# Optimization experiments

Measured on AMD Instinct MI355X. Metric: run time of the kernel, lower is better.

The kernel has to match this reference:

```python
import jax, jax.numpy as jnp
import numpy as np

N, E, IN_C, HID, OUT_C = 100000, 1600000, 256, 64, 64
K, ALPHA, LN_EPS = 10, 0.1, 1e-5


def _layernorm(h, gamma, beta):
    mu = jnp.mean(h, axis=-1, keepdims=True)
    var = jnp.var(h, axis=-1, keepdims=True)
    return (h - mu) * jax.lax.rsqrt(var + LN_EPS) * gamma + beta


def _appnp(h, edge_index):
    # gcn_norm with added self-loops (fill value 1), symmetric normalization
    n = h.shape[0]
    sl = jnp.arange(n)
    row = jnp.concatenate([edge_index[0], sl])
    col = jnp.concatenate([edge_index[1], sl])
    w = jnp.ones(row.shape[0], dtype=h.dtype)
    deg = jax.ops.segment_sum(w, col, num_segments=n)
    dinv = jnp.where(deg > 0, jax.lax.rsqrt(deg), 0.0)
    norm = dinv[row] * w * dinv[col]  # [E+N]
    h0 = h
    for _ in range(K):
        msg = norm[:, None] * h[row]                       # gather [E+N, HID]
        agg = jax.ops.segment_sum(msg, col, num_segments=n)  # scatter-add
        h = (1.0 - ALPHA) * agg + ALPHA * h0
    return h


def setup_inputs() -> dict:
    key = jax.random.key(0)
    ks = jax.random.split(key, 8)
    x = jax.random.normal(ks[0], (N, IN_C), dtype=jnp.float32)
    edge_index = jax.random.randint(ks[1], (2, E), 0, N, dtype=jnp.int64)
    W1 = jax.random.normal(ks[2], (IN_C, HID), dtype=jnp.float32) / np.sqrt(IN_C)
    b1 = jnp.zeros((HID,), dtype=jnp.float32)
    g1 = jnp.ones((HID,), dtype=jnp.float32)
    be1 = jnp.zeros((HID,), dtype=jnp.float32)
    g2 = jnp.ones((HID,), dtype=jnp.float32)
    be2 = jnp.zeros((HID,), dtype=jnp.float32)
    W2 = jax.random.normal(ks[3], (HID, OUT_C), dtype=jnp.float32) / np.sqrt(HID)
    b2 = jnp.zeros((OUT_C,), dtype=jnp.float32)
    return {"x": x, "edge_index": edge_index, "W1": W1, "b1": b1,
            "g1": g1, "be1": be1, "g2": g2, "be2": be2, "W2": W2, "b2": b2}


def reference(x, edge_index, W1, b1, g1, be1, g2, be2, W2, b2):
    h = jax.nn.gelu(x @ W1 + b1, approximate=False)   # Linear + exact GELU (torch default)
    h = _layernorm(h, g1, be1)
    h = jax.nn.gelu(_appnp(h, edge_index), approximate=False)
    h = _layernorm(h, g2, be2)
    # dropout inactive in eval mode
    return h @ W2 + b2
```

## Files before the change

### kernel.cpp

```cpp
#include <hip/hip_runtime.h>
#include <math.h>

#define HID 64
#define INC 256
#define LN_EPS 1e-5f
#define ALPHA 0.1f
#define NBKT 256
#define BCAP 12288

typedef unsigned short ushort_t;
typedef unsigned int uint_t;
using short8v = __attribute__((ext_vector_type(8))) short;
using float4v = __attribute__((ext_vector_type(4))) float;

__device__ __forceinline__ float gelu_exact(float x) {
    return 0.5f * x * (1.0f + erff(x * 0.70710678118654752f));
}

__device__ __forceinline__ float wave_sum64(float v) {
#pragma unroll
    for (int m = 1; m < 64; m <<= 1) v += __shfl_xor(v, m, 64);
    return v;
}

__device__ __forceinline__ ushort_t f2bf(float f) {
    uint_t u = __float_as_uint(f);
    return (ushort_t)((u + 0x7fffu + ((u >> 16) & 1u)) >> 16);
}
__device__ __forceinline__ float bf_lo(uint_t v) { return __uint_as_float(v << 16); }
__device__ __forceinline__ float bf_hi(uint_t v) { return __uint_as_float(v & 0xffff0000u); }

__device__ __forceinline__ void split_bf(float f, ushort_t& hi, ushort_t& lo) {
    uint_t ub = __float_as_uint(f);
    uint_t h = (ub + 0x7fffu + ((ub >> 16) & 1u)) >> 16;
    hi = (ushort_t)h;
    float fl = f - __uint_as_float(h << 16);
    uint_t lb = __float_as_uint(fl);
    lo = (ushort_t)((lb + 0x7fffu + ((lb >> 16) & 1u)) >> 16);
}

__global__ __launch_bounds__(256) void k_prepW(const float* __restrict__ W1,
                                               ushort_t* __restrict__ whi,
                                               ushort_t* __restrict__ wlo) {
    int e = blockIdx.x * 256 + threadIdx.x;
    int col = e & 63, k = e >> 6;
    float f = W1[(size_t)k * HID + col];
    ushort_t hi, lo;
    split_bf(f, hi, lo);
    int idx = col * 256 + (((k >> 3) ^ (col & 7)) << 3) + (k & 7);
    whi[idx] = hi;
    wlo[idx] = lo;
}

__global__ __launch_bounds__(256) void k_prepW2(const float* __restrict__ W2,
                                                ushort_t* __restrict__ whi,
                                                ushort_t* __restrict__ wlo) {
    int e = blockIdx.x * 256 + threadIdx.x;
    int col = e & 63, k = e >> 6;
    float f = W2[(size_t)k * HID + col];
    ushort_t hi, lo;
    split_bf(f, hi, lo);
    int idx = col * 64 + (((k >> 3) ^ (col & 7)) << 3) + (k & 7);
    whi[idx] = hi;
    wlo[idx] = lo;
}

__global__ __launch_bounds__(256) void k_bin(const int* __restrict__ ei,
                                             int* __restrict__ bcur,
                                             uint_t* __restrict__ binned, int E) {
    __shared__ int hist[NBKT];
    __shared__ int base[NBKT];
    const int t = threadIdx.x;
    const int c0 = blockIdx.x * 4096;
    hist[t] = 0;
    __syncthreads();
#pragma unroll
    for (int i = 0; i < 16; ++i) {
        int e = c0 + i * 256 + t;
        if (e < E) atomicAdd(&hist[ei[E + e] >> 9], 1);
    }
    __syncthreads();
    {
        int h = hist[t];
        base[t] = (h > 0) ? atomicAdd(&bcur[t], h) : 0;
        hist[t] = 0;
    }
    __syncthreads();
#pragma unroll
    for (int i = 0; i < 16; ++i) {
        int e = c0 + i * 256 + t;
        if (e < E) {
            int src = ei[e];
            int dst = ei[E + e];
            int b = dst >> 9;
            int r = atomicAdd(&hist[b], 1);
            int pos = base[b] + r;
            if (pos >= BCAP) pos = BCAP - 1;
            binned[(size_t)b * BCAP + pos] = (uint_t)src | ((uint_t)(dst & 511) << 20);
        }
    }
}

__global__ __launch_bounds__(256) void k_csrA(const uint_t* __restrict__ binned,
                                              const int* __restrict__ bcur,
                                              int* __restrict__ cnt,
                                              float* __restrict__ dinv,
                                              int* __restrict__ offl,
                                              int* __restrict__ bpad, int N) {
    __shared__ int cl[512];
    __shared__ int ps[256];
    const int b = blockIdx.x, t = threadIdx.x;
    const int nE = bcur[b];
    const uint_t* be = binned + (size_t)b * BCAP;
    cl[t] = 0;
    cl[t + 256] = 0;
    __syncthreads();
    for (int i = t; i < nE; i += 256) atomicAdd(&cl[be[i] >> 20], 1);
    __syncthreads();
    const int ca = cl[2 * t], cb = cl[2 * t + 1];
    const int p4a = (ca + 3) & ~3, p4b = (cb + 3) & ~3;
    const int p = p4a + p4b;
    ps[t] = p;
    __syncthreads();
#pragma unroll
    for (int o = 1; o < 256; o <<= 1) {
        int add = (t >= o) ? ps[t - o] : 0;
        __syncthreads();
        ps[t] += add;
        __syncthreads();
    }
    const int pbase = ps[t] - p;
    const int g0 = b * 512 + 2 * t;
    if (g0 < N) {
        cnt[g0] = ca;
        dinv[g0] = rsqrtf((float)(ca + 1));
        offl[g0] = pbase;
    }
    if (g0 + 1 < N) {
        cnt[g0 + 1] = cb;
        dinv[g0 + 1] = rsqrtf((float)(cb + 1));
        offl[g0 + 1] = pbase + p4a;
    }
    if (t == 255) bpad[b] = ps[255];
}

__global__ __launch_bounds__(256) void k_bktscan(const int* __restrict__ bpad,
                                                 int* __restrict__ bbase,
                                                 int* __restrict__ rowstart, int N) {
    __shared__ int s[256];
    const int t = threadIdx.x;
    const int v = bpad[t];
    s[t] = v;
    __syncthreads();
#pragma unroll
    for (int off = 1; off < 256; off <<= 1) {
        int add = (t >= off) ? s[t - off] : 0;
        __syncthreads();
        s[t] += add;
        __syncthreads();
    }
    bbase[t] = s[t] - v;
    if (t == 255) rowstart[N] = s[255];
}

__global__ __launch_bounds__(256) void k_csrB(const uint_t* __restrict__ binned,
                                              const int* __restrict__ bcur,
                                              const int* __restrict__ bbase,
                                              const int* __restrict__ offl,
                                              const int* __restrict__ cnt,
                                              int* __restrict__ csr,
                                              int* __restrict__ rowstart, int N) {
    __shared__ int st[512];
    __shared__ int cur[512];
    const int b = blockIdx.x, t = threadIdx.x;
    const int nE = bcur[b];
    const int gb = bbase[b];
    const uint_t* be = binned + (size_t)b * BCAP;
    const int n0 = b * 512;
    for (int i = t; i < 512; i += 256) {
        int g = n0 + i;
        int s = (g < N) ? gb + offl[g] : 0;
        st[i] = s;
        cur[i] = s;
        if (g < N) rowstart[g] = s;
    }
    __syncthreads();
    for (int i = t; i < nE; i += 256) {
        uint_t rec = be[i];
        int ln = rec >> 20;
        int r = atomicAdd(&cur[ln], 1);
        csr[r] = (int)(rec & 0xFFFFFu);
    }
    __syncthreads();
    for (int i = t; i < 512; i += 256) {
        int g = n0 + i;
        if (g < N) {
            int c = cnt[g];
            int end = st[i] + ((c + 3) & ~3);
            for (int j = st[i] + c; j < end; ++j) csr[j] = N;
        }
    }
}

__global__ __launch_bounds__(512, 4) void k_gemm1ln(const float* __restrict__ x,
                                                    const ushort_t* __restrict__ whi,
                                                    const ushort_t* __restrict__ wlo,
                                                    const float* __restrict__ b1,
                                                    const float* __restrict__ g1,
                                                    const float* __restrict__ be1,
                                                    const float* __restrict__ dinv,
                                                    ushort_t* __restrict__ u0, int N) {
    __shared__ ushort_t Wh[16384];
    __shared__ ushort_t Wl[16384];
    const int t = threadIdx.x;
    {
        const uint4* s1 = (const uint4*)whi;
        uint4* d1 = (uint4*)Wh;
        for (int i = t; i < 2048; i += 512) d1[i] = s1[i];
        const uint4* s2 = (const uint4*)wlo;
        uint4* d2 = (uint4*)Wl;
        for (int i = t; i < 2048; i += 512) d2[i] = s2[i];
    }

    const int lane = t & 63, w = t >> 6;
    const int l15 = lane & 15, lg = lane >> 4;
    const int row0 = blockIdx.x * 128 + w * 16;
    int rowc = row0 + l15;
    if (rowc > N - 1) rowc = N - 1;
    const float* xr = x + (size_t)rowc * INC + lg * 8;

    float4 ax[16];
#pragma unroll
    for (int i = 0; i < 8; ++i) {
        ax[2 * i] = *(const float4*)(xr + i * 32);
        ax[2 * i + 1] = *(const float4*)(xr + i * 32 + 4);
    }
    __syncthreads();

    float4v acc[4];
#pragma unroll
    for (int i = 0; i < 4; ++i) acc[i] = (float4v){0.f, 0.f, 0.f, 0.f};

    union U8 { short8v v; ushort_t u[8]; };

#pragma unroll
    for (int t8 = 0; t8 < 8; ++t8) {
        U8 ahi, alo;
        {
            const float af[8] = {ax[2 * t8].x, ax[2 * t8].y, ax[2 * t8].z, ax[2 * t8].w,
                                 ax[2 * t8 + 1].x, ax[2 * t8 + 1].y, ax[2 * t8 + 1].z,
                                 ax[2 * t8 + 1].w};
#pragma unroll
            for (int j = 0; j < 8; ++j) split_bf(af[j], ahi.u[j], alo.u[j]);
        }
        const int kb = t8 * 4 + lg;
#pragma unroll
        for (int ct = 0; ct < 4; ++ct) {
            const int col = ct * 16 + l15;
            const int idx = col * 256 + ((kb ^ (col & 7)) << 3);
            const short8v bhi = *(const short8v*)&Wh[idx];
            const short8v blo = *(const short8v*)&Wl[idx];
            acc[ct] = __builtin_amdgcn_mfma_f32_16x16x32_bf16(ahi.v, bhi, acc[ct], 0, 0, 0);
            acc[ct] = __builtin_amdgcn_mfma_f32_16x16x32_bf16(ahi.v, blo, acc[ct], 0, 0, 0);
            acc[ct] = __builtin_amdgcn_mfma_f32_16x16x32_bf16(alo.v, bhi, acc[ct], 0, 0, 0);
        }
    }

    float b1c[4], g1c[4], bec[4];
#pragma unroll
    for (int ct = 0; ct < 4; ++ct) {
        const int col = ct * 16 + l15;
        b1c[ct] = b1[col];
        g1c[ct] = g1[col];
        bec[ct] = be1[col];
    }
    float gv[4][4];
#pragma unroll
    for (int ct = 0; ct < 4; ++ct)
#pragma unroll
        for (int r = 0; r < 4; ++r) gv[ct][r] = gelu_exact(acc[ct][r] + b1c[ct]);

    float mu[4], rsv[4];
#pragma unroll
    for (int r = 0; r < 4; ++r) {
        float p = gv[0][r] + gv[1][r] + gv[2][r] + gv[3][r];
        p += __shfl_xor(p, 1, 64);
        p += __shfl_xor(p, 2, 64);
        p += __shfl_xor(p, 4, 64);
        p += __shfl_xor(p, 8, 64);
        mu[r] = p * (1.0f / 64.0f);
        float d0 = gv[0][r] - mu[r], d1 = gv[1][r] - mu[r];
        float d2 = gv[2][r] - mu[r], d3 = gv[3][r] - mu[r];
        float p2 = d0 * d0 + d1 * d1 + d2 * d2 + d3 * d3;
        p2 += __shfl_xor(p2, 1, 64);
        p2 += __shfl_xor(p2, 2, 64);
        p2 += __shfl_xor(p2, 4, 64);
        p2 += __shfl_xor(p2, 8, 64);
        rsv[r] = rsqrtf(p2 * (1.0f / 64.0f) + LN_EPS);
    }
#pragma unroll
    for (int r = 0; r < 4; ++r) {
        const int row = row0 + lg * 4 + r;
        if (row < N) {
            const float di = dinv[row];
#pragma unroll
            for (int ct = 0; ct < 4; ++ct) {
                const float ln = (gv[ct][r] - mu[r]) * rsv[r] * g1c[ct] + bec[ct];
                u0[(size_t)row * HID + ct * 16 + l15] = f2bf(di * ln);
            }
        }
    }
}

__global__ __launch_bounds__(256) void k_prop(const ushort_t* __restrict__ uin,
                                              const ushort_t* __restrict__ u0,
                                              ushort_t* __restrict__ uout,
                                              const int* __restrict__ csr,
                                              const int* __restrict__ rowstart,
                                              const float* __restrict__ dinv, int N) {
    const int t = threadIdx.x;
    const int lane = t & 63;
    const int q = lane >> 4, fl = lane & 15;
    const int node = blockIdx.x * 4 + (t >> 6);
    if (node >= N) return;
    const uint2* U = (const uint2*)uin;
    const int s0 = rowstart[node];
    const int e1 = rowstart[node + 1];
    float a0 = 0.f, a1 = 0.f, a2 = 0.f, a3 = 0.f;
    for (int e = s0; e < e1; e += 16) {
        const int ge = e + 4 * q;
        int4 id = make_int4(N, N, N, N);
        if (ge < e1) id = *(const int4*)(csr + ge);
        const uint2 v0 = U[(size_t)id.x * 16 + fl];
        const uint2 v1 = U[(size_t)id.y * 16 + fl];
        const uint2 v2 = U[(size_t)id.z * 16 + fl];
        const uint2 v3 = U[(size_t)id.w * 16 + fl];
        a0 += bf_lo(v0.x) + bf_lo(v1.x) + bf_lo(v2.x) + bf_lo(v3.x);
        a1 += bf_hi(v0.x) + bf_hi(v1.x) + bf_hi(v2.x) + bf_hi(v3.x);
        a2 += bf_lo(v0.y) + bf_lo(v1.y) + bf_lo(v2.y) + bf_lo(v3.y);
        a3 += bf_hi(v0.y) + bf_hi(v1.y) + bf_hi(v2.y) + bf_hi(v3.y);
    }
    a0 += __shfl_xor(a0, 16, 64); a0 += __shfl_xor(a0, 32, 64);
    a1 += __shfl_xor(a1, 16, 64); a1 += __shfl_xor(a1, 32, 64);
    a2 += __shfl_xor(a2, 16, 64); a2 += __shfl_xor(a2, 32, 64);
    a3 += __shfl_xor(a3, 16, 64); a3 += __shfl_xor(a3, 32, 64);
    if (lane < 16) {
        const uint2 ud = U[(size_t)node * 16 + fl];
        const uint2 uz = ((const uint2*)u0)[(size_t)node * 16 + fl];
        const float di = dinv[node];
        const float c = (1.0f - ALPHA) * di * di;
        const float r0 = c * (a0 + bf_lo(ud.x)) + ALPHA * bf_lo(uz.x);
        const float r1 = c * (a1 + bf_hi(ud.x)) + ALPHA * bf_hi(uz.x);
        const float r2 = c * (a2 + bf_lo(ud.y)) + ALPHA * bf_lo(uz.y);
        const float r3 = c * (a3 + bf_hi(ud.y)) + ALPHA * bf_hi(uz.y);
        uint2 o;
        o.x = (uint_t)f2bf(r0) | ((uint_t)f2bf(r1) << 16);
        o.y = (uint_t)f2bf(r2) | ((uint_t)f2bf(r3) << 16);
        ((uint2*)uout)[(size_t)node * 16 + fl] = o;
    }
}

__global__ __launch_bounds__(256) void k_final(const ushort_t* __restrict__ u,
                                               const int* __restrict__ cnt,
                                               const float* __restrict__ g2,
                                               const float* __restrict__ be2,
                                               const ushort_t* __restrict__ w2hi,
                                               const ushort_t* __restrict__ w2lo,
                                               const float* __restrict__ b2,
                                               float* __restrict__ out, int N) {
    __shared__ ushort_t Wh[4096];
    __shared__ ushort_t Wl[4096];
    const int t = threadIdx.x;
    {
        const uint4* s1 = (const uint4*)w2hi;
        uint4* d1 = (uint4*)Wh;
        for (int i = t; i < 512; i += 256) d1[i] = s1[i];
        const uint4* s2 = (const uint4*)w2lo;
        uint4* d2 = (uint4*)Wl;
        for (int i = t; i < 512; i += 256) d2[i] = s2[i];
    }
    __syncthreads();

    const int lane = t & 63, w = t >> 6;
    const int l15 = lane & 15, lg = lane >> 4;
    const int row0 = blockIdx.x * 64 + w * 16;
    if (row0 >= N) return;
    int rowc = row0 + l15;
    if (rowc > N - 1) rowc = N - 1;

    const uint4 uva = *(const uint4*)(u + (size_t)rowc * HID + lg * 8);
    const uint4 uvb = *(const uint4*)(u + (size_t)rowc * HID + 32 + lg * 8);
    const float sc = sqrtf((float)(cnt[rowc] + 1));

    float v[16];
    {
        const uint_t ua_[4] = {uva.x, uva.y, uva.z, uva.w};
        const uint_t ub_[4] = {uvb.x, uvb.y, uvb.z, uvb.w};
#pragma unroll
        for (int j = 0; j < 4; ++j) {
            v[2 * j] = gelu_exact(bf_lo(ua_[j]) * sc);
            v[2 * j + 1] = gelu_exact(bf_hi(ua_[j]) * sc);
            v[8 + 2 * j] = gelu_exact(bf_lo(ub_[j]) * sc);
            v[8 + 2 * j + 1] = gelu_exact(bf_hi(ub_[j]) * sc);
        }
    }
    float s = 0.f;
#pragma unroll
    for (int j = 0; j < 16; ++j) s += v[j];
    s += __shfl_xor(s, 16, 64);
    s += __shfl_xor(s, 32, 64);
    const float mu = s * (1.0f / 64.0f);
    float sq = 0.f;
#pragma unroll
    for (int j = 0; j < 16; ++j) {
        v[j] -= mu;
        sq += v[j] * v[j];
    }
    sq += __shfl_xor(sq, 16, 64);
    sq += __shfl_xor(sq, 32, 64);
    const float rs = rsqrtf(sq * (1.0f / 64.0f) + LN_EPS);

    union U8 { short8v v; ushort_t u[8]; };
    U8 a0, a1;
#pragma unroll
    for (int j = 0; j < 8; ++j) {
        const int ka = lg * 8 + j;
        const int kb = 32 + lg * 8 + j;
        a0.u[j] = f2bf(v[j] * rs * g2[ka] + be2[ka]);
        a1.u[j] = f2bf(v[8 + j] * rs * g2[kb] + be2[kb]);
    }

    float4v acc[4];
#pragma unroll
    for (int i = 0; i < 4; ++i) acc[i] = (float4v){0.f, 0.f, 0.f, 0.f};
#pragma unroll
    for (int ct = 0; ct < 4; ++ct) {
        const int col = ct * 16 + l15;
        const int i0 = col * 64 + ((lg ^ (col & 7)) << 3);
        const int i1 = col * 64 + (((4 + lg) ^ (col & 7)) << 3);
        short8v b0h = *(const short8v*)&Wh[i0];
        short8v b0l = *(const short8v*)&Wl[i0];
        short8v b1h = *(const short8v*)&Wh[i1];
        short8v b1l = *(const short8v*)&Wl[i1];
        acc[ct] = __builtin_amdgcn_mfma_f32_16x16x32_bf16(a0.v, b0h, acc[ct], 0, 0, 0);
        acc[ct] = __builtin_amdgcn_mfma_f32_16x16x32_bf16(a0.v, b0l, acc[ct], 0, 0, 0);
        acc[ct] = __builtin_amdgcn_mfma_f32_16x16x32_bf16(a1.v, b1h, acc[ct], 0, 0, 0);
        acc[ct] = __builtin_amdgcn_mfma_f32_16x16x32_bf16(a1.v, b1l, acc[ct], 0, 0, 0);
    }

#pragma unroll
    for (int ct = 0; ct < 4; ++ct) {
        const float bb = b2[ct * 16 + l15];
#pragma unroll
        for (int r = 0; r < 4; ++r) {
            const int row = row0 + lg * 4 + r;
            if (row < N) out[(size_t)row * HID + ct * 16 + l15] = acc[ct][r] + bb;
        }
    }
}

extern "C" void kernel_launch(void* const* d_in, const int* in_sizes, int n_in,
                              void* d_out, int out_size, void* d_ws, size_t ws_size,
                              hipStream_t stream) {
    const float* x   = (const float*)d_in[0];
    const int*   ei  = (const int*)d_in[1];
    const float* W1  = (const float*)d_in[2];
    const float* b1  = (const float*)d_in[3];
    const float* g1  = (const float*)d_in[4];
    const float* be1 = (const float*)d_in[5];
    const float* g2  = (const float*)d_in[6];
    const float* be2 = (const float*)d_in[7];
    const float* W2  = (const float*)d_in[8];
    const float* b2  = (const float*)d_in[9];
    float* out = (float*)d_out;

    const int N = in_sizes[0] / INC;
    const int E = in_sizes[1] / 2;

    char* ws = (char*)d_ws;
    size_t o = 0;
    auto alloc = [&](size_t bytes) { size_t r = o; o += (bytes + 255) & ~(size_t)255; return r; };
    ushort_t* u0 = (ushort_t*)(ws + alloc((size_t)(N + 1) * HID * 2));
    ushort_t* ua = (ushort_t*)(ws + alloc((size_t)(N + 1) * HID * 2));
    ushort_t* ub = (ushort_t*)(ws + alloc((size_t)(N + 1) * HID * 2));
    float* dinv     = (float*)(ws + alloc((size_t)N * 4));
    int*   cnt      = (int*)(ws + alloc((size_t)N * 4));
    int*   offl     = (int*)(ws + alloc((size_t)N * 4));
    int*   rowstart = (int*)(ws + alloc((size_t)(N + 1) * 4));
    int*   bcur     = (int*)(ws + alloc(NBKT * 4));
    int*   bpad     = (int*)(ws + alloc(NBKT * 4));
    int*   bbase    = (int*)(ws + alloc(NBKT * 4));
    ushort_t* whi   = (ushort_t*)(ws + alloc(16384 * 2));
    ushort_t* wlo   = (ushort_t*)(ws + alloc(16384 * 2));
    ushort_t* w2hi  = (ushort_t*)(ws + alloc(4096 * 2));
    ushort_t* w2lo  = (ushort_t*)(ws + alloc(4096 * 2));
    uint_t* binned  = (uint_t*)(ws + alloc((size_t)NBKT * BCAP * 4));
    int*   csr      = (int*)(ws + alloc((size_t)(E + 3 * (size_t)N + 256) * 4));

    const int nbkt = (N + 511) / 512;

    hipMemsetAsync(bcur, 0, NBKT * 4, stream);
    hipMemsetAsync(bpad, 0, NBKT * 4, stream);
    hipMemsetAsync(u0 + (size_t)N * HID, 0, HID * 2, stream);
    hipMemsetAsync(ua + (size_t)N * HID, 0, HID * 2, stream);
    hipMemsetAsync(ub + (size_t)N * HID, 0, HID * 2, stream);

    k_prepW<<<64, 256, 0, stream>>>(W1, whi, wlo);
    k_prepW2<<<16, 256, 0, stream>>>(W2, w2hi, w2lo);
    k_bin<<<(E + 4095) / 4096, 256, 0, stream>>>(ei, bcur, binned, E);
    k_csrA<<<nbkt, 256, 0, stream>>>(binned, bcur, cnt, dinv, offl, bpad, N);
    k_bktscan<<<1, 256, 0, stream>>>(bpad, bbase, rowstart, N);
    k_csrB<<<nbkt, 256, 0, stream>>>(binned, bcur, bbase, offl, cnt, csr, rowstart, N);
    k_gemm1ln<<<(N + 127) / 128, 512, 0, stream>>>(x, whi, wlo, b1, g1, be1, dinv, u0, N);

    ushort_t* bufs[2] = {ua, ub};
    const ushort_t* pin = u0;
    for (int k = 0; k < 10; ++k) {
        ushort_t* pout = bufs[k & 1];
        k_prop<<<(N + 3) / 4, 256, 0, stream>>>(pin, u0, pout, csr, rowstart, dinv, N);
        pin = pout;
    }
    k_final<<<(N + 63) / 64, 256, 0, stream>>>(pin, cnt, g2, be2, w2hi, w2lo, b2, out, N);
}
```

Measured before the change: 537.1 us.

## Shard feature matrix into four 16-column slabs for cache-local propagation gathers

```diff
diff --git a/kernel.cpp b/kernel.cpp
--- a/kernel.cpp
+++ b/kernel.cpp
@@ -15,12 +15,6 @@
 
 __device__ __forceinline__ float gelu_exact(float x) {
     return 0.5f * x * (1.0f + erff(x * 0.70710678118654752f));
-}
-
-__device__ __forceinline__ float wave_sum64(float v) {
-#pragma unroll
-    for (int m = 1; m < 64; m <<= 1) v += __shfl_xor(v, m, 64);
-    return v;
 }
 
 __device__ __forceinline__ ushort_t f2bf(float f) {
@@ -63,6 +57,17 @@
     int idx = col * 64 + (((k >> 3) ^ (col & 7)) << 3) + (k & 7);
     whi[idx] = hi;
     wlo[idx] = lo;
+}
+
+__global__ void k_zero(ushort_t* __restrict__ u0, ushort_t* __restrict__ ua,
+                       ushort_t* __restrict__ ub, int N) {
+    const int t = threadIdx.x;
+    if (t < 192) {
+        ushort_t* bufs[3] = {u0, ua, ub};
+        ushort_t* p = bufs[t >> 6];
+        const int shard = (t & 63) >> 4, f = t & 15;
+        p[((size_t)shard * (N + 1) + N) * 16 + f] = 0;
+    }
 }
 
 __global__ __launch_bounds__(256) void k_bin(const int* __restrict__ ei,
@@ -306,7 +311,7 @@
 #pragma unroll
             for (int ct = 0; ct < 4; ++ct) {
                 const float ln = (gv[ct][r] - mu[r]) * rsv[r] * g1c[ct] + bec[ct];
-                u0[(size_t)row * HID + ct * 16 + l15] = f2bf(di * ln);
+                u0[((size_t)ct * (N + 1) + row) * 16 + l15] = f2bf(di * ln);
             }
         }
     }
@@ -317,36 +322,42 @@
                                               ushort_t* __restrict__ uout,
                                               const int* __restrict__ csr,
                                               const int* __restrict__ rowstart,
-                                              const float* __restrict__ dinv, int N) {
+                                              const float* __restrict__ dinv,
+                                              int N, int nbl) {
+    const int blk = blockIdx.x;
+    const int g = blk & 7;
+    const int shard = g >> 1;
+    const int nb = ((blk >> 3) << 1) + (g & 1);
+    if (nb >= nbl) return;
     const int t = threadIdx.x;
-    const int lane = t & 63;
-    const int q = lane >> 4, fl = lane & 15;
-    const int node = blockIdx.x * 4 + (t >> 6);
-    if (node >= N) return;
-    const uint2* U = (const uint2*)uin;
-    const int s0 = rowstart[node];
-    const int e1 = rowstart[node + 1];
+    const int lane = t & 63, w = t >> 6;
+    const int nl = lane >> 4;
+    const int es = (lane >> 2) & 3;
+    const int fl = lane & 3;
+    const int node = nb * 16 + w * 4 + nl;
+    const bool valid = node < N;
+    const uint2* Us = (const uint2*)uin + (size_t)shard * (N + 1) * 4;
+    int s0 = 0, e1 = 0;
+    if (valid) {
+        s0 = rowstart[node];
+        e1 = rowstart[node + 1];
+    }
     float a0 = 0.f, a1 = 0.f, a2 = 0.f, a3 = 0.f;
-    for (int e = s0; e < e1; e += 16) {
-        const int ge = e + 4 * q;
-        int4 id = make_int4(N, N, N, N);
-        if (ge < e1) id = *(const int4*)(csr + ge);
-        const uint2 v0 = U[(size_t)id.x * 16 + fl];
-        const uint2 v1 = U[(size_t)id.y * 16 + fl];
-        const uint2 v2 = U[(size_t)id.z * 16 + fl];
-        const uint2 v3 = U[(size_t)id.w * 16 + fl];
-        a0 += bf_lo(v0.x) + bf_lo(v1.x) + bf_lo(v2.x) + bf_lo(v3.x);
-        a1 += bf_hi(v0.x) + bf_hi(v1.x) + bf_hi(v2.x) + bf_hi(v3.x);
-        a2 += bf_lo(v0.y) + bf_lo(v1.y) + bf_lo(v2.y) + bf_lo(v3.y);
-        a3 += bf_hi(v0.y) + bf_hi(v1.y) + bf_hi(v2.y) + bf_hi(v3.y);
-    }
-    a0 += __shfl_xor(a0, 16, 64); a0 += __shfl_xor(a0, 32, 64);
-    a1 += __shfl_xor(a1, 16, 64); a1 += __shfl_xor(a1, 32, 64);
-    a2 += __shfl_xor(a2, 16, 64); a2 += __shfl_xor(a2, 32, 64);
-    a3 += __shfl_xor(a3, 16, 64); a3 += __shfl_xor(a3, 32, 64);
-    if (lane < 16) {
-        const uint2 ud = U[(size_t)node * 16 + fl];
-        const uint2 uz = ((const uint2*)u0)[(size_t)node * 16 + fl];
+    for (int e = s0 + es; e < e1; e += 4) {
+        const int idx = csr[e];
+        const uint2 v = Us[(size_t)idx * 4 + fl];
+        a0 += bf_lo(v.x);
+        a1 += bf_hi(v.x);
+        a2 += bf_lo(v.y);
+        a3 += bf_hi(v.y);
+    }
+    a0 += __shfl_xor(a0, 4, 64); a0 += __shfl_xor(a0, 8, 64);
+    a1 += __shfl_xor(a1, 4, 64); a1 += __shfl_xor(a1, 8, 64);
+    a2 += __shfl_xor(a2, 4, 64); a2 += __shfl_xor(a2, 8, 64);
+    a3 += __shfl_xor(a3, 4, 64); a3 += __shfl_xor(a3, 8, 64);
+    if (valid && es == 0) {
+        const uint2 ud = Us[(size_t)node * 4 + fl];
+        const uint2 uz = ((const uint2*)u0 + (size_t)shard * (N + 1) * 4)[(size_t)node * 4 + fl];
         const float di = dinv[node];
         const float c = (1.0f - ALPHA) * di * di;
         const float r0 = c * (a0 + bf_lo(ud.x)) + ALPHA * bf_lo(uz.x);
@@ -356,7 +367,7 @@
         uint2 o;
         o.x = (uint_t)f2bf(r0) | ((uint_t)f2bf(r1) << 16);
         o.y = (uint_t)f2bf(r2) | ((uint_t)f2bf(r3) << 16);
-        ((uint2*)uout)[(size_t)node * 16 + fl] = o;
+        ((uint2*)uout + (size_t)shard * (N + 1) * 4)[(size_t)node * 4 + fl] = o;
     }
 }
 
@@ -388,8 +399,9 @@
     int rowc = row0 + l15;
     if (rowc > N - 1) rowc = N - 1;
 
-    const uint4 uva = *(const uint4*)(u + (size_t)rowc * HID + lg * 8);
-    const uint4 uvb = *(const uint4*)(u + (size_t)rowc * HID + 32 + lg * 8);
+    const int oA = (lg & 1) * 8;
+    const uint4 uva = *(const uint4*)(u + ((size_t)(lg >> 1) * (N + 1) + rowc) * 16 + oA);
+    const uint4 uvb = *(const uint4*)(u + ((size_t)(2 + (lg >> 1)) * (N + 1) + rowc) * 16 + oA);
     const float sc = sqrtf((float)(cnt[rowc] + 1));
 
     float v[16];
@@ -498,13 +510,13 @@
     int*   csr      = (int*)(ws + alloc((size_t)(E + 3 * (size_t)N + 256) * 4));
 
     const int nbkt = (N + 511) / 512;
+    const int nbl = (N + 15) / 16;
+    const int propGrid = 8 * ((nbl + 1) / 2);
 
     hipMemsetAsync(bcur, 0, NBKT * 4, stream);
     hipMemsetAsync(bpad, 0, NBKT * 4, stream);
-    hipMemsetAsync(u0 + (size_t)N * HID, 0, HID * 2, stream);
-    hipMemsetAsync(ua + (size_t)N * HID, 0, HID * 2, stream);
-    hipMemsetAsync(ub + (size_t)N * HID, 0, HID * 2, stream);
-
+
+    k_zero<<<1, 256, 0, stream>>>(u0, ua, ub, N);
     k_prepW<<<64, 256, 0, stream>>>(W1, whi, wlo);
     k_prepW2<<<16, 256, 0, stream>>>(W2, w2hi, w2lo);
     k_bin<<<(E + 4095) / 4096, 256, 0, stream>>>(ei, bcur, binned, E);
@@ -517,7 +529,7 @@
     const ushort_t* pin = u0;
     for (int k = 0; k < 10; ++k) {
         ushort_t* pout = bufs[k & 1];
-        k_prop<<<(N + 3) / 4, 256, 0, stream>>>(pin, u0, pout, csr, rowstart, dinv, N);
+        k_prop<<<propGrid, 256, 0, stream>>>(pin, u0, pout, csr, rowstart, dinv, N, nbl);
         pin = pout;
     }
     k_final<<<(N + 63) / 64, 256, 0, stream>>>(pin, cnt, g2, be2, w2hi, w2lo, b2, out, N);
```

After: 751.7 us. +40.0%, slower.
